# Optimization experiments

Measured on AMD Instinct MI355X. Metric: run time of the kernel, lower is better.

## Reference

```python
import jax, jax.numpy as jnp
import numpy as np

B, R, L, K = 64, 196, 512, 768
NEG = jnp.float32(-2**31 + 1)


def setup_inputs() -> dict:
    key = jax.random.key(0)
    ks = jax.random.split(key, 8)
    image_emb = jax.random.normal(ks[0], (B, R, L), dtype=jnp.float32)
    seq_emb = jax.random.normal(ks[1], (B, L, K), dtype=jnp.float32)
    mask = jax.random.randint(ks[2], (B, L), 0, 2, dtype=jnp.int32)
    # Linear(l,1) and Linear(k,1) params, Xavier-ish scale
    image_W = jax.random.normal(ks[3], (L, 1), dtype=jnp.float32) / np.sqrt(L)
    image_b = jnp.zeros((1,), dtype=jnp.float32)
    seq_W = jax.random.normal(ks[4], (K, 1), dtype=jnp.float32) / np.sqrt(K)
    seq_b = jnp.zeros((1,), dtype=jnp.float32)
    # V_weight [L, L], xavier_uniform
    lim = np.sqrt(6.0 / (L + L)).astype(np.float32)
    V_weight = jax.random.uniform(ks[5], (L, L), dtype=jnp.float32, minval=-lim, maxval=lim)
    return {"image_emb": image_emb, "seq_emb": seq_emb, "mask": mask,
            "image_W": image_W, "image_b": image_b,
            "seq_W": seq_W, "seq_b": seq_b, "V_weight": V_weight}


def reference(image_emb, seq_emb, mask, image_W, image_b, seq_W, seq_b, V_weight):
    # p: [B,R,1], q: [B,L,1]
    p = jnp.tanh(image_emb @ image_W + image_b)
    q = jnp.tanh(seq_emb @ seq_W + seq_b)
    qt = jnp.swapaxes(q, 1, 2)              # [B,1,L]
    emb = p @ qt + qt                       # [B,R,L] (rank-1 outer + broadcast add)
    score = emb @ V_weight                  # [B,R,L]
    # dropout_rate=0.0 -> identity
    score = jnp.where(mask[:, None, :] == 0, NEG, score)
    score = jax.nn.softmax(score, axis=-1)  # [B,R,L]
    out = score @ seq_emb                   # [B,R,K]
    out = out / jnp.sqrt(jnp.float32(seq_emb.shape[-1]))
    return out
```

## Files before the change

kernel.cpp:

```cpp
#include <hip/hip_runtime.h>
#include <cstdint>
#include <cstddef>


typedef __attribute__((ext_vector_type(8))) short short8;
typedef __attribute__((ext_vector_type(4))) float f32x4;

__device__ __forceinline__ unsigned short f32_to_bf16(float x) {
    unsigned int u = __float_as_uint(x);
    unsigned int r = (u + 0x7FFFu + ((u >> 16) & 1u)) >> 16;
    return (unsigned short)r;
}
__device__ __forceinline__ float bf16_to_f32(unsigned short h) {
    return __uint_as_float(((unsigned int)h) << 16);
}

__global__ __launch_bounds__(256) void krows_p(const float* __restrict__ x,
                                               const float* __restrict__ w,
                                               const float* __restrict__ bias,
                                               float* __restrict__ outp) {
    int wv = threadIdx.x >> 6, lane = threadIdx.x & 63;
    int row = blockIdx.x * 4 + wv;
    const float4* x4 = (const float4*)(x + (size_t)row * 512);
    const float4* w4 = (const float4*)w;
    float s = 0.f;
#pragma unroll
    for (int i = 0; i < 2; ++i) {
        float4 a = x4[i * 64 + lane];
        float4 c = w4[i * 64 + lane];
        s += a.x * c.x + a.y * c.y + a.z * c.z + a.w * c.w;
    }
#pragma unroll
    for (int o = 32; o; o >>= 1) s += __shfl_xor(s, o, 64);
    if (lane == 0) outp[row] = tanhf(s + bias[0]);
}

__global__ __launch_bounds__(256) void krows_q(const float* __restrict__ x,
                                               const float* __restrict__ w,
                                               const float* __restrict__ bias,
                                               float* __restrict__ outp) {
    int wv = threadIdx.x >> 6, lane = threadIdx.x & 63;
    int row = blockIdx.x * 4 + wv;
    const float4* x4 = (const float4*)(x + (size_t)row * 768);
    const float4* w4 = (const float4*)w;
    float s = 0.f;
#pragma unroll
    for (int i = 0; i < 3; ++i) {
        float4 a = x4[i * 64 + lane];
        float4 c = w4[i * 64 + lane];
        s += a.x * c.x + a.y * c.y + a.z * c.z + a.w * c.w;
    }
#pragma unroll
    for (int o = 32; o; o >>= 1) s += __shfl_xor(s, o, 64);
    if (lane == 0) outp[row] = tanhf(s + bias[0]);
}

__global__ __launch_bounds__(256) void ktrans(const float* __restrict__ seq,
                                              const float* __restrict__ seqW,
                                              const float* __restrict__ bias,
                                              unsigned short* __restrict__ seqT,
                                              float* __restrict__ qv) {
    __shared__ __align__(16) float sW[768];
    __shared__ __align__(16) unsigned short sT[128 * 74];
    int b = blockIdx.x >> 3, jt = blockIdx.x & 7;
    int j0 = jt * 64;
    int t = threadIdx.x;
    sW[t] = seqW[t]; sW[t + 256] = seqW[t + 256]; sW[t + 512] = seqW[t + 512];
    int rowin = t >> 5, seg = t & 31;
    const float* base = seq + (size_t)b * 512 * 768 + (size_t)j0 * 768;
    unsigned short* dstb0 = seqT + (size_t)b * 768 * 512 + j0;
    int kr8 = t >> 3, jseg = t & 7;
    float qp[8] = {0.f, 0.f, 0.f, 0.f, 0.f, 0.f, 0.f, 0.f};
    __syncthreads();
    for (int ck = 0; ck < 6; ++ck) {
        if (ck) __syncthreads();
#pragma unroll
        for (int p = 0; p < 8; ++p) {
            int jl = p * 8 + rowin;
            float4 a = *(const float4*)(base + (size_t)jl * 768 + ck * 128 + seg * 4);
            float4 w = *(const float4*)(sW + ck * 128 + seg * 4);
            qp[p] += a.x * w.x + a.y * w.y + a.z * w.z + a.w * w.w;
            int c0 = seg * 4;
            sT[(c0 + 0) * 74 + jl] = f32_to_bf16(a.x);
            sT[(c0 + 1) * 74 + jl] = f32_to_bf16(a.y);
            sT[(c0 + 2) * 74 + jl] = f32_to_bf16(a.z);
            sT[(c0 + 3) * 74 + jl] = f32_to_bf16(a.w);
        }
        __syncthreads();
        const unsigned int* sT32 = (const unsigned int*)sT;
        unsigned short* dstb = dstb0 + (size_t)ck * 128 * 512;
#pragma unroll
        for (int wp = 0; wp < 4; ++wp) {
            int kr = wp * 32 + kr8;
            uint4 v;
            v.x = sT32[kr * 37 + jseg * 4 + 0];
            v.y = sT32[kr * 37 + jseg * 4 + 1];
            v.z = sT32[kr * 37 + jseg * 4 + 2];
            v.w = sT32[kr * 37 + jseg * 4 + 3];
            *(uint4*)(dstb + (size_t)kr * 512 + jseg * 8) = v;
        }
    }
#pragma unroll
    for (int p = 0; p < 8; ++p) {
        float s = qp[p];
#pragma unroll
        for (int o = 16; o; o >>= 1) s += __shfl_xor(s, o, 64);
        if ((t & 31) == 0) qv[b * 512 + j0 + p * 8 + rowin] = tanhf(s + bias[0]);
    }
}

__global__ __launch_bounds__(256) void kw(const float* __restrict__ qv,
                                          const float* __restrict__ V,
                                          const int* __restrict__ mask,
                                          float* __restrict__ wm) {
    __shared__ __align__(16) float sq[512];
    __shared__ __align__(16) float sacc[8][32][4];
    int b = blockIdx.x >> 2, jc = blockIdx.x & 3;
    int t = threadIdx.x;
    sq[t] = qv[b * 512 + t];
    sq[t + 256] = qv[b * 512 + t + 256];
    __syncthreads();
    int jt = t & 31, lg = t >> 5;
    const float4* V4 = (const float4*)V;
    int col4 = jc * 32 + jt;
    float ax = 0.f, ay = 0.f, az = 0.f, aw = 0.f;
    int lbase = lg * 64;
#pragma unroll 8
    for (int li = 0; li < 64; ++li) {
        int l = lbase + li;
        float qq = sq[l];
        float4 v = V4[(size_t)l * 128 + col4];
        ax += qq * v.x; ay += qq * v.y; az += qq * v.z; aw += qq * v.w;
    }
    sacc[lg][jt][0] = ax; sacc[lg][jt][1] = ay;
    sacc[lg][jt][2] = az; sacc[lg][jt][3] = aw;
    __syncthreads();
    if (t < 32) {
        float sx = 0.f, sy = 0.f, sz = 0.f, sw = 0.f;
#pragma unroll
        for (int g = 0; g < 8; ++g) {
            sx += sacc[g][t][0]; sy += sacc[g][t][1];
            sz += sacc[g][t][2]; sw += sacc[g][t][3];
        }
        const int* mrow = mask + b * 512 + jc * 128 + t * 4;
        float4 o;
        o.x = mrow[0] ? sx : -1e30f;
        o.y = mrow[1] ? sy : -1e30f;
        o.z = mrow[2] ? sz : -1e30f;
        o.w = mrow[3] ? sw : -1e30f;
        ((float4*)(wm + b * 512 + jc * 128))[t] = o;
    }
}

__global__ __launch_bounds__(256, 2) void kattn2(const unsigned short* __restrict__ seqT,
                                                 const float* __restrict__ p,
                                                 const float* __restrict__ wm,
                                                 float* __restrict__ out) {
    __shared__ __align__(16) unsigned short sB[2][128 * 64];
    __shared__ __align__(16) float swm[512];
    __shared__ float sinvz[64];
    __shared__ float sred[16];

    int raw = blockIdx.x;
    int g  = ((raw >> 5) << 3) + (raw & 7);
    int rt = (raw >> 3) & 3;
    int b  = g / 6, nt = g - b * 6;
    int t  = threadIdx.x;
    int wv = t >> 6, lane = t & 63;
    int mm = lane & 15, q = lane >> 4;
    int nb = nt * 128;

    float v0 = wm[b * 512 + t];
    float v1 = wm[b * 512 + t + 256];
    swm[t] = v0; swm[t + 256] = v1;
    float lmax = fmaxf(v0, v1);
    float fa = (v0 > -1e29f) ? v0 : 1e30f;
    float fb = (v1 > -1e29f) ? v1 : 1e30f;
    float lmin = fminf(fa, fb);
#pragma unroll
    for (int o = 32; o; o >>= 1) {
        lmax = fmaxf(lmax, __shfl_xor(lmax, o, 64));
        lmin = fminf(lmin, __shfl_xor(lmin, o, 64));
    }
    if (lane == 0) { sred[wv] = lmax; sred[8 + wv] = lmin; }
    __syncthreads();
    float wmax = fmaxf(fmaxf(sred[0], sred[1]), fmaxf(sred[2], sred[3]));
    float wmin = fminf(fminf(sred[8], sred[9]), fminf(sred[10], sred[11]));

    int rl = wv * 16 + mm;
    int r  = rt * 64 + rl;
    bool valid = r < 196;
    int pidx = b * 196 + (valid ? r : 195);
    float c = 1.0f + p[pidx];
    float M = (c >= 0.f) ? c * wmax : c * wmin;

    short8 afrag[16];
    float zsum = 0.f;
    const f32x4* swm4 = (const f32x4*)swm;
#pragma unroll
    for (int tk = 0; tk < 16; ++tk) {
        int jb = tk * 32 + q * 8;
        f32x4 w0 = swm4[jb >> 2];
        f32x4 w1 = swm4[(jb >> 2) + 1];
        short8 af;
#pragma unroll
        for (int jj = 0; jj < 8; ++jj) {
            float ww = (jj < 4) ? w0[jj] : w1[jj - 4];
            float e = valid ? __expf(c * ww - M) : 0.f;
            unsigned short h = f32_to_bf16(e);
            zsum += bf16_to_f32(h);
            af[jj] = (short)h;
        }
        afrag[tk] = af;
    }
    zsum += __shfl_xor(zsum, 16, 64);
    zsum += __shfl_xor(zsum, 32, 64);
    if (q == 0) sinvz[rl] = 1.0f / zsum;

    f32x4 acc[8];
#pragma unroll
    for (int s = 0; s < 8; ++s) acc[s] = (f32x4){0.f, 0.f, 0.f, 0.f};

    const unsigned short* seqTb = seqT + (size_t)b * 768 * 512 + (size_t)nb * 512;
    int nrow = t >> 3, jg = t & 7;
    auto stage = [&](int ch, int buf) {
        unsigned short* sb = sB[buf];
#pragma unroll
        for (int pp = 0; pp < 4; ++pp) {
            int n = pp * 32 + nrow;
            short8 v = *(const short8*)(seqTb + (size_t)n * 512 + ch * 64 + jg * 8);
            int sw = (n ^ (n >> 3)) & 7;
            *(short8*)(sb + n * 64 + ((jg ^ sw) << 3)) = v;
        }
    };

    __syncthreads();
    stage(0, 0);
    __syncthreads();
#pragma unroll
    for (int ch = 0; ch < 8; ++ch) {
        if (ch < 7) stage(ch + 1, (ch + 1) & 1);
        const unsigned short* cb = sB[ch & 1];
#pragma unroll
        for (int kk = 0; kk < 2; ++kk) {
            short8 bfr[8];
#pragma unroll
            for (int s = 0; s < 8; ++s) {
                int n = s * 16 + mm;
                int sw = (n ^ (n >> 3)) & 7;
                bfr[s] = *(const short8*)(cb + n * 64 + ((((kk << 2) + q) ^ sw) << 3));
            }
#pragma unroll
            for (int s = 0; s < 8; ++s)
                acc[s] = __builtin_amdgcn_mfma_f32_16x16x32_bf16(
                    afrag[(ch << 1) + kk], bfr[s], acc[s], 0, 0, 0);
        }
        __syncthreads();
    }

    const float invsqrtk = 0.036084391824351615f;
#pragma unroll
    for (int reg = 0; reg < 4; ++reg) {
        int row = q * 4 + reg;
        int rr = rt * 64 + wv * 16 + row;
        if (rr < 196) {
            float scale = sinvz[wv * 16 + row] * invsqrtk;
            float* op = out + (size_t)(b * 196 + rr) * 768 + nb + mm;
#pragma unroll
            for (int s = 0; s < 8; ++s)
                op[s * 16] = acc[s][reg] * scale;
        }
    }
}

__global__ __launch_bounds__(256, 2) void kattn(const float* __restrict__ seq,
                                                const float* __restrict__ p,
                                                const float* __restrict__ wm,
                                                float* __restrict__ out) {
    __shared__ __align__(16) unsigned int sseq[2][128 * 32];
    __shared__ __align__(16) float swm[512];
    __shared__ float sinvz[64];
    __shared__ float sred[16];

    int id = blockIdx.x;
    int rt = id & 3;
    int nt = (id >> 2) % 6;
    int b  = id / 24;
    int t  = threadIdx.x;
    int wv = t >> 6, lane = t & 63;
    int mm = lane & 15, q = lane >> 4;
    int nb = nt * 128;

    float v0 = wm[b * 512 + t];
    float v1 = wm[b * 512 + t + 256];
    swm[t] = v0; swm[t + 256] = v1;
    float lmax = fmaxf(v0, v1);
    float fa = (v0 > -1e29f) ? v0 : 1e30f;
    float fb = (v1 > -1e29f) ? v1 : 1e30f;
    float lmin = fminf(fa, fb);
#pragma unroll
    for (int o = 32; o; o >>= 1) {
        lmax = fmaxf(lmax, __shfl_xor(lmax, o, 64));
        lmin = fminf(lmin, __shfl_xor(lmin, o, 64));
    }
    if (lane == 0) { sred[wv] = lmax; sred[8 + wv] = lmin; }
    __syncthreads();
    float wmax = fmaxf(fmaxf(sred[0], sred[1]), fmaxf(sred[2], sred[3]));
    float wmin = fminf(fminf(sred[8], sred[9]), fminf(sred[10], sred[11]));

    int rl = wv * 16 + mm;
    int r  = rt * 64 + rl;
    bool valid = r < 196;
    int pidx = b * 196 + (valid ? r : 195);
    float c = 1.0f + p[pidx];
    float M = (c >= 0.f) ? c * wmax : c * wmin;

    short8 afrag[16];
    float zsum = 0.f;
    const f32x4* swm4 = (const f32x4*)swm;
#pragma unroll
    for (int tk = 0; tk < 16; ++tk) {
        int jb = tk * 32 + q * 8;
        f32x4 w0 = swm4[jb >> 2];
        f32x4 w1 = swm4[(jb >> 2) + 1];
        short8 af;
#pragma unroll
        for (int jj = 0; jj < 8; ++jj) {
            float ww = (jj < 4) ? w0[jj] : w1[jj - 4];
            float e = valid ? __expf(c * ww - M) : 0.f;
            unsigned short h = f32_to_bf16(e);
            zsum += bf16_to_f32(h);
            af[jj] = (short)h;
        }
        afrag[tk] = af;
    }
    zsum += __shfl_xor(zsum, 16, 64);
    zsum += __shfl_xor(zsum, 32, 64);
    if (q == 0) sinvz[rl] = 1.0f / zsum;

    f32x4 acc[8];
#pragma unroll
    for (int s = 0; s < 8; ++s) acc[s] = (f32x4){0.f, 0.f, 0.f, 0.f};

    const float* seqb = seq + (size_t)b * 512 * 768 + nb;
    int tl = t & 31, jp = t >> 5;
    int n0 = tl * 4;
    auto stage = [&](int ch, int buf) {
        unsigned int* sb = sseq[buf];
#pragma unroll
        for (int pass = 0; pass < 4; ++pass) {
            int jl = pass * 16 + jp * 2;
            int jglob = ch * 64 + jl;
            float4 a0 = *(const float4*)(seqb + (size_t)jglob * 768 + n0);
            float4 a1 = *(const float4*)(seqb + (size_t)(jglob + 1) * 768 + n0);
            float a0v[4] = {a0.x, a0.y, a0.z, a0.w};
            float a1v[4] = {a1.x, a1.y, a1.z, a1.w};
            int g = jl >> 3;
            int wo = (jl & 7) >> 1;
#pragma unroll
            for (int i = 0; i < 4; ++i) {
                int n = n0 + i;
                int sw = (n ^ (n >> 3)) & 7;
                unsigned int pk = (unsigned int)f32_to_bf16(a0v[i]) |
                                  ((unsigned int)f32_to_bf16(a1v[i]) << 16);
                sb[n * 32 + ((g ^ sw) << 2) + wo] = pk;
            }
        }
    };

    __syncthreads();
    stage(0, 0);
    __syncthreads();
#pragma unroll
    for (int ch = 0; ch < 8; ++ch) {
        if (ch < 7) stage(ch + 1, (ch + 1) & 1);
        const unsigned int* cb = sseq[ch & 1];
#pragma unroll
        for (int kk = 0; kk < 2; ++kk) {
            short8 bfr[8];
#pragma unroll
            for (int s = 0; s < 8; ++s) {
                int n = s * 16 + mm;
                int g = kk * 4 + q;
                int sw = (n ^ (n >> 3)) & 7;
                bfr[s] = *(const short8*)(cb + n * 32 + ((g ^ sw) << 2));
            }
#pragma unroll
            for (int s = 0; s < 8; ++s)
                acc[s] = __builtin_amdgcn_mfma_f32_16x16x32_bf16(
                    afrag[ch * 2 + kk], bfr[s], acc[s], 0, 0, 0);
        }
        __syncthreads();
    }

    const float invsqrtk = 0.036084391824351615f;
#pragma unroll
    for (int reg = 0; reg < 4; ++reg) {
        int row = q * 4 + reg;
        int rr = rt * 64 + wv * 16 + row;
        if (rr < 196) {
            float scale = sinvz[wv * 16 + row] * invsqrtk;
            float* op = out + (size_t)(b * 196 + rr) * 768 + nb + mm;
#pragma unroll
            for (int s = 0; s < 8; ++s)
                op[s * 16] = acc[s][reg] * scale;
        }
    }
}

extern "C" void kernel_launch(void* const* d_in, const int* in_sizes, int n_in,
                              void* d_out, int out_size, void* d_ws, size_t ws_size,
                              hipStream_t stream) {
    const float* image_emb = (const float*)d_in[0];
    const float* seq_emb   = (const float*)d_in[1];
    const int*   mask      = (const int*)d_in[2];
    const float* image_W   = (const float*)d_in[3];
    const float* image_b   = (const float*)d_in[4];
    const float* seq_W     = (const float*)d_in[5];
    const float* seq_b     = (const float*)d_in[6];
    const float* V         = (const float*)d_in[7];
    float* out = (float*)d_out;

    float* p_ws  = (float*)d_ws;
    float* q_ws  = (float*)((char*)d_ws + (64 << 10));
    float* wm_ws = (float*)((char*)d_ws + (192 << 10));
    unsigned short* seqT = (unsigned short*)((char*)d_ws + (384 << 10));

    size_t need = (size_t)(384 << 10) + (size_t)64 * 768 * 512 * 2;
    krows_p<<<dim3(3136), dim3(256), 0, stream>>>(image_emb, image_W, image_b, p_ws);
    if (ws_size >= need) {
        ktrans<<<dim3(512), dim3(256), 0, stream>>>(seq_emb, seq_W, seq_b, seqT, q_ws);
        kw<<<dim3(256), dim3(256), 0, stream>>>(q_ws, V, mask, wm_ws);
        kattn2<<<dim3(1536), dim3(256), 0, stream>>>(seqT, p_ws, wm_ws, out);
    } else {
        krows_q<<<dim3(8192), dim3(256), 0, stream>>>(seq_emb, seq_W, seq_b, q_ws);
        kw<<<dim3(256), dim3(256), 0, stream>>>(q_ws, V, mask, wm_ws);
        kattn<<<dim3(1536), dim3(256), 0, stream>>>(seq_emb, p_ws, wm_ws, out);
    }
}
```

Baseline: 242.6 us.

## Fuse image projection into transpose kernel with swizzled LDS and packed bf16 converts

Merges the image-row projection kernel (krows_p) into the seq transpose/projection kernel as extra blocks, removing one kernel launch. The transpose is restructured so each thread loads four rows and packs pairs of bf16 values with a hardware packed-convert builtin. Transposed data is written to LDS as 64-bit words using an XOR swizzle in place of scalar 16-bit stores into a padded array. This aims to cut LDS store count and bank conflicts, at the cost of more complex indexing and a heterogeneous grid.

```diff
diff --git a/kernel.cpp b/kernel.cpp
--- a/kernel.cpp
+++ b/kernel.cpp
@@ -13,6 +13,120 @@
 }
 __device__ __forceinline__ float bf16_to_f32(unsigned short h) {
     return __uint_as_float(((unsigned int)h) << 16);
+}
+
+#if defined(__has_builtin)
+#if __has_builtin(__builtin_amdgcn_cvt_pk_bf16_f32)
+#define HAVE_PK_BF16 1
+#endif
+#endif
+
+__device__ __forceinline__ unsigned int pk_bf16(float a, float b) {
+#ifdef HAVE_PK_BF16
+    typedef __attribute__((ext_vector_type(2))) __bf16 bf16x2;
+    bf16x2 v = __builtin_amdgcn_cvt_pk_bf16_f32(a, b);
+    return __builtin_bit_cast(unsigned int, v);
+#else
+    return (unsigned int)f32_to_bf16(a) | ((unsigned int)f32_to_bf16(b) << 16);
+#endif
+}
+
+__global__ __launch_bounds__(256) void kprep(const float* __restrict__ seq,
+                                             const float* __restrict__ seqW,
+                                             const float* __restrict__ seqBias,
+                                             const float* __restrict__ img,
+                                             const float* __restrict__ imgW,
+                                             const float* __restrict__ imgBias,
+                                             unsigned short* __restrict__ seqT,
+                                             float* __restrict__ qv,
+                                             float* __restrict__ pv) {
+    __shared__ __align__(16) unsigned int sT[128 * 32];
+    __shared__ __align__(16) float sW[768];
+
+    if (blockIdx.x >= 512) {
+        int wv = threadIdx.x >> 6, lane = threadIdx.x & 63;
+        int row = (blockIdx.x - 512) * 4 + wv;
+        const float4* x4 = (const float4*)(img + (size_t)row * 512);
+        const float4* w4 = (const float4*)imgW;
+        float s = 0.f;
+#pragma unroll
+        for (int i = 0; i < 2; ++i) {
+            float4 a = x4[i * 64 + lane];
+            float4 c = w4[i * 64 + lane];
+            s += a.x * c.x + a.y * c.y + a.z * c.z + a.w * c.w;
+        }
+#pragma unroll
+        for (int o = 32; o; o >>= 1) s += __shfl_xor(s, o, 64);
+        if (lane == 0) pv[row] = tanhf(s + imgBias[0]);
+        return;
+    }
+
+    int b = blockIdx.x >> 3, jt = blockIdx.x & 7;
+    int j0 = jt * 64;
+    int t = threadIdx.x;
+    sW[t] = seqW[t]; sW[t + 256] = seqW[t + 256]; sW[t + 512] = seqW[t + 512];
+
+    int quad = t >> 4, kseg = t & 15;
+    int qk = quad ^ kseg;
+    const float* base = seq + (size_t)b * 512 * 768 + (size_t)(j0 + quad * 4) * 768;
+    int jg = t & 7, krow = t >> 3;
+    unsigned short* dst0 = seqT + (size_t)b * 768 * 512 + j0;
+    float qp[4] = {0.f, 0.f, 0.f, 0.f};
+    __syncthreads();
+
+    for (int ck = 0; ck < 6; ++ck) {
+        if (ck) __syncthreads();
+#pragma unroll
+        for (int rp = 0; rp < 2; ++rp) {
+            int kq = rp * 64 + kseg * 4;
+            int kg = ck * 128 + kq;
+            float4 r0 = *(const float4*)(base + 0 * 768 + kg);
+            float4 r1 = *(const float4*)(base + 1 * 768 + kg);
+            float4 r2 = *(const float4*)(base + 2 * 768 + kg);
+            float4 r3 = *(const float4*)(base + 3 * 768 + kg);
+            float4 w  = *(const float4*)(sW + kg);
+            qp[0] += r0.x * w.x + r0.y * w.y + r0.z * w.z + r0.w * w.w;
+            qp[1] += r1.x * w.x + r1.y * w.y + r1.z * w.z + r1.w * w.w;
+            qp[2] += r2.x * w.x + r2.y * w.y + r2.z * w.z + r2.w * w.w;
+            qp[3] += r3.x * w.x + r3.y * w.y + r3.z * w.z + r3.w * w.w;
+            float a0[4] = {r0.x, r0.y, r0.z, r0.w};
+            float a1[4] = {r1.x, r1.y, r1.z, r1.w};
+            float a2[4] = {r2.x, r2.y, r2.z, r2.w};
+            float a3[4] = {r3.x, r3.y, r3.z, r3.w};
+#pragma unroll
+            for (int i = 0; i < 4; ++i) {
+                int k = kq + i;
+                int col = (qk ^ (i << 2)) & 15;
+                uint2 v;
+                v.x = pk_bf16(a0[i], a1[i]);
+                v.y = pk_bf16(a2[i], a3[i]);
+                *(uint2*)(sT + k * 32 + col * 2) = v;
+            }
+        }
+        __syncthreads();
+        unsigned short* dst = dst0 + (size_t)ck * 128 * 512;
+#pragma unroll
+        for (int wp = 0; wp < 4; ++wp) {
+            int k = wp * 32 + krow;
+            int s = ((k >> 2) & 15) ^ ((k & 3) << 2);
+            int c0 = ((jg << 1) ^ s) & 15;
+            int c1 = ((jg << 1) ^ 1 ^ s) & 15;
+            uint2 va = *(const uint2*)(sT + k * 32 + c0 * 2);
+            uint2 vb = *(const uint2*)(sT + k * 32 + c1 * 2);
+            uint4 o;
+            o.x = va.x; o.y = va.y; o.z = vb.x; o.w = vb.y;
+            *(uint4*)(dst + (size_t)k * 512 + jg * 8) = o;
+        }
+    }
+#pragma unroll
+    for (int rr = 0; rr < 4; ++rr) {
+        float s = qp[rr];
+        s += __shfl_xor(s, 8, 64);
+        s += __shfl_xor(s, 4, 64);
+        s += __shfl_xor(s, 2, 64);
+        s += __shfl_xor(s, 1, 64);
+        if (kseg == 0) qv[b * 512 + j0 + quad * 4 + rr] = tanhf(s + seqBias[0]);
+    }
 }
 
 __global__ __launch_bounds__(256) void krows_p(const float* __restrict__ x,
@@ -53,60 +167,6 @@
 #pragma unroll
     for (int o = 32; o; o >>= 1) s += __shfl_xor(s, o, 64);
     if (lane == 0) outp[row] = tanhf(s + bias[0]);
-}
-
-__global__ __launch_bounds__(256) void ktrans(const float* __restrict__ seq,
-                                              const float* __restrict__ seqW,
-                                              const float* __restrict__ bias,
-                                              unsigned short* __restrict__ seqT,
-                                              float* __restrict__ qv) {
-    __shared__ __align__(16) float sW[768];
-    __shared__ __align__(16) unsigned short sT[128 * 74];
-    int b = blockIdx.x >> 3, jt = blockIdx.x & 7;
-    int j0 = jt * 64;
-    int t = threadIdx.x;
-    sW[t] = seqW[t]; sW[t + 256] = seqW[t + 256]; sW[t + 512] = seqW[t + 512];
-    int rowin = t >> 5, seg = t & 31;
-    const float* base = seq + (size_t)b * 512 * 768 + (size_t)j0 * 768;
-    unsigned short* dstb0 = seqT + (size_t)b * 768 * 512 + j0;
-    int kr8 = t >> 3, jseg = t & 7;
-    float qp[8] = {0.f, 0.f, 0.f, 0.f, 0.f, 0.f, 0.f, 0.f};
-    __syncthreads();
-    for (int ck = 0; ck < 6; ++ck) {
-        if (ck) __syncthreads();
-#pragma unroll
-        for (int p = 0; p < 8; ++p) {
-            int jl = p * 8 + rowin;
-            float4 a = *(const float4*)(base + (size_t)jl * 768 + ck * 128 + seg * 4);
-            float4 w = *(const float4*)(sW + ck * 128 + seg * 4);
-            qp[p] += a.x * w.x + a.y * w.y + a.z * w.z + a.w * w.w;
-            int c0 = seg * 4;
-            sT[(c0 + 0) * 74 + jl] = f32_to_bf16(a.x);
-            sT[(c0 + 1) * 74 + jl] = f32_to_bf16(a.y);
-            sT[(c0 + 2) * 74 + jl] = f32_to_bf16(a.z);
-            sT[(c0 + 3) * 74 + jl] = f32_to_bf16(a.w);
-        }
-        __syncthreads();
-        const unsigned int* sT32 = (const unsigned int*)sT;
-        unsigned short* dstb = dstb0 + (size_t)ck * 128 * 512;
-#pragma unroll
-        for (int wp = 0; wp < 4; ++wp) {
-            int kr = wp * 32 + kr8;
-            uint4 v;
-            v.x = sT32[kr * 37 + jseg * 4 + 0];
-            v.y = sT32[kr * 37 + jseg * 4 + 1];
-            v.z = sT32[kr * 37 + jseg * 4 + 2];
-            v.w = sT32[kr * 37 + jseg * 4 + 3];
-            *(uint4*)(dstb + (size_t)kr * 512 + jseg * 8) = v;
-        }
-    }
-#pragma unroll
-    for (int p = 0; p < 8; ++p) {
-        float s = qp[p];
-#pragma unroll
-        for (int o = 16; o; o >>= 1) s += __shfl_xor(s, o, 64);
-        if ((t & 31) == 0) qv[b * 512 + j0 + p * 8 + rowin] = tanhf(s + bias[0]);
-    }
 }
 
 __global__ __launch_bounds__(256) void kw(const float* __restrict__ qv,
@@ -427,12 +487,14 @@
     unsigned short* seqT = (unsigned short*)((char*)d_ws + (384 << 10));
 
     size_t need = (size_t)(384 << 10) + (size_t)64 * 768 * 512 * 2;
-    krows_p<<<dim3(3136), dim3(256), 0, stream>>>(image_emb, image_W, image_b, p_ws);
     if (ws_size >= need) {
-        ktrans<<<dim3(512), dim3(256), 0, stream>>>(seq_emb, seq_W, seq_b, seqT, q_ws);
+        kprep<<<dim3(3648), dim3(256), 0, stream>>>(seq_emb, seq_W, seq_b,
+                                                    image_emb, image_W, image_b,
+                                                    seqT, q_ws, p_ws);
         kw<<<dim3(256), dim3(256), 0, stream>>>(q_ws, V, mask, wm_ws);
         kattn2<<<dim3(1536), dim3(256), 0, stream>>>(seqT, p_ws, wm_ws, out);
     } else {
+        krows_p<<<dim3(3136), dim3(256), 0, stream>>>(image_emb, image_W, image_b, p_ws);
         krows_q<<<dim3(8192), dim3(256), 0, stream>>>(seq_emb, seq_W, seq_b, q_ws);
         kw<<<dim3(256), dim3(256), 0, stream>>>(q_ws, V, mask, wm_ws);
         kattn<<<dim3(1536), dim3(256), 0, stream>>>(seq_emb, p_ws, wm_ws, out);
```

Measured after the change: 239.1 us. About the same (-1.5%).
